# Kernel tuning notes

Measured on AMD Instinct MI355X. Metric: run time of the kernel, lower is better.

Reference implementation:

```python
import jax, jax.numpy as jnp
import numpy as np

WP = 1.0     # warp_penalty
TEMP = 0.01  # soft-min temperature
BIG = 1e7    # finite stand-in for +inf (exp(-BIG/TEMP) == 0 exactly in fp32)


def setup_inputs() -> dict:
    key = jax.random.key(0)
    k1, k2, k3, k4 = jax.random.split(key, 4)
    B, T1, T2, C = 8, 256, 1024, 128
    fea_a = jax.random.normal(k1, (B, T1, C), jnp.float32)
    fea_b = jax.random.normal(k2, (B, T2, C), jnp.float32)
    len_a = jax.random.randint(k3, (B,), T1 // 2, T1 + 1)
    len_b = jax.random.randint(k4, (B,), T2 // 2, T2 + 1)
    return {"fea_a": fea_a, "len_a": len_a, "fea_b": fea_b, "len_b": len_b}


def _softmin(v, temp):
    # v: [3, B, T1]; stable -temp*log(sum(exp(-v/temp)))
    m = jnp.min(v, axis=0)
    return m - temp * jnp.log(jnp.sum(jnp.exp(-(v - m) / temp), axis=0))


def _soft_dtw(fea_a, fea_b, len_a, len_b, wp=WP, temp=TEMP):
    B, T1, C = fea_a.shape
    T2 = fea_b.shape[1]
    # L1 cost: [B, T2, T1]  (rows index fea_b, cols index fea_a, as in torch code)
    cost = jnp.mean(jnp.abs(fea_a[:, None, :, :] - fea_b[:, :, None, :]), axis=-1)
    # skewed cost: skew[b, d, j] = cost[b, clip(d-j, 0, T2-1), j]
    D = T1 + T2 - 1
    d = jnp.arange(D)[:, None]
    j = jnp.arange(T1)[None, :]
    idx = jnp.clip(d - j, 0, T2 - 1)           # [D, T1]
    skew = cost[:, idx, j]                      # [B, D, T1]
    skew = jnp.swapaxes(skew, 0, 1)             # [D, B, T1] for scan

    pc0 = jnp.full((B, T1 + 1), BIG, jnp.float32)       # path_cost (diag d-1)
    pcp0 = pc0.at[:, 0].set(0.0)                         # path_cost_prev (diag d-2)

    def step(carry, crow):
        pc, pcp = carry
        dirs = jnp.stack([pcp[:, :-1], pc[:, 1:] + wp, pc[:, :-1] + wp], axis=0)
        new = crow + _softmin(dirs, temp)                # [B, T1]
        new = jnp.concatenate([jnp.full((B, 1), BIG, new.dtype), new], axis=1)
        return (new, pc), new

    _, ys = jax.lax.scan(step, (pc0, pcp0), skew)        # ys: [D, B, T1+1]
    # per-sample answer: diagonal len_a+len_b-2, entry len_a
    di = len_a + len_b - 2
    loss_i = ys[di, jnp.arange(B), len_a]
    return jnp.sum(loss_i)  # reduction='mean' over a length-1 accumulator == sum


def reference(fea_a, len_a, fea_b, len_b):
    return _soft_dtw(fea_a, fea_b, len_a, len_b)
```

## Files before the change

kernel.cpp:

```cpp
#include <hip/hip_runtime.h>
#include <hip/hip_bf16.h>
#include <hip/hip_fp16.h>
#include <cstddef>
#include <cstdint>

#define BIGV 10000000.0f
#define WPV  1.0f

#define BATCH 8
#define T1N 256
#define T2N 1024
#define CN 128
#define DN 1279

#define RPB 16
#define NSLOT 3
#define SLOT_BYTES (RPB * 1024)
#define FLAG_MAGIC 0x600D0000

typedef __attribute__((ext_vector_type(2))) _Float16 half2v;

__global__ __launch_bounds__(256) void cost_kernel(const float* __restrict__ A,
                                                   const float* __restrict__ Bf,
                                                   const int* __restrict__ lenA,
                                                   const int* __restrict__ lenB,
                                                   float* __restrict__ sk) {
    __shared__ char As[64 * 256];
    __shared__ char Bs[127 * 256];

    const int b  = blockIdx.z;
    const int d0 = blockIdx.y * 64;
    const int j0 = blockIdx.x * 64;
    const int tid = threadIdx.x;

    const int dEnd = lenA[b] + lenB[b] - 2;
    if (d0 > dEnd) return;

    const float* Ab = A  + (size_t)b * T1N * CN;
    const float* Bb = Bf + (size_t)b * T2N * CN;

    const int tj = tid & 15;
    const int td = tid >> 4;
    const int brow0 = td - tj + 63;
    const int rbase = d0 - j0 - 63;

#define SWB(row, g) (((row) << 8) + ((((g) + (row)) & 15) << 4))

    #pragma unroll
    for (int i = 0; i < 8; ++i) {
        int idx = tid + i * 256;
        int row = idx >> 5;
        int q   = idx & 31;
        float4 f = *(const float4*)(Ab + (size_t)(j0 + row) * CN + (q << 2));
        half2v h0 = { (_Float16)f.x, (_Float16)f.y };
        half2v h1 = { (_Float16)f.z, (_Float16)f.w };
        char* dst = As + SWB(row, q >> 1) + ((q & 1) << 3);
        ((uint32_t*)dst)[0] = __builtin_bit_cast(uint32_t, h0);
        ((uint32_t*)dst)[1] = __builtin_bit_cast(uint32_t, h1);
    }
    #pragma unroll
    for (int i = 0; i < 16; ++i) {
        int idx = tid + i * 256;
        if (idx < 4064) {
            int row = idx >> 5;
            int q   = idx & 31;
            int gr = rbase + row;
            gr = gr < 0 ? 0 : (gr > T2N - 1 ? T2N - 1 : gr);
            float4 f = *(const float4*)(Bb + (size_t)gr * CN + (q << 2));
            half2v h0 = { (_Float16)f.x, (_Float16)f.y };
            half2v h1 = { (_Float16)f.z, (_Float16)f.w };
            char* dst = Bs + SWB(row, q >> 1) + ((q & 1) << 3);
            ((uint32_t*)dst)[0] = __builtin_bit_cast(uint32_t, h0);
            ((uint32_t*)dst)[1] = __builtin_bit_cast(uint32_t, h1);
        }
    }
    __syncthreads();

    float acc[4][4];
    #pragma unroll
    for (int i = 0; i < 4; ++i)
        #pragma unroll
        for (int j = 0; j < 4; ++j) acc[i][j] = 0.0f;

    const half2v one2 = { (_Float16)1.0f, (_Float16)1.0f };

    for (int g = 0; g < 16; ++g) {
        uint4 a4[4], bv[7];
        #pragma unroll
        for (int ji = 0; ji < 4; ++ji) {
            int row = tj + 16 * ji;
            a4[ji] = *(const uint4*)(As + SWB(row, g));
        }
        #pragma unroll
        for (int m = 0; m < 7; ++m) {
            int row = brow0 + 16 * (m - 3);
            bv[m] = *(const uint4*)(Bs + SWB(row, g));
        }
        #pragma unroll
        for (int dk = 0; dk < 4; ++dk) {
            #pragma unroll
            for (int ji = 0; ji < 4; ++ji) {
                uint4 au = a4[ji];
                uint4 bu = bv[dk - ji + 3];
                float a = acc[dk][ji];
                #pragma unroll
                for (int w = 0; w < 4; ++w) {
                    uint32_t ua = (&au.x)[w];
                    uint32_t ub = (&bu.x)[w];
                    half2v d2 = __builtin_bit_cast(half2v, ua)
                              - __builtin_bit_cast(half2v, ub);
                    uint32_t du = __builtin_bit_cast(uint32_t, d2) & 0x7FFF7FFFu;
#if __has_builtin(__builtin_amdgcn_fdot2)
                    a = __builtin_amdgcn_fdot2(__builtin_bit_cast(half2v, du),
                                               one2, a, false);
#else
                    half2v ad = __builtin_bit_cast(half2v, du);
                    a += (float)ad.x + (float)ad.y;
#endif
                }
                acc[dk][ji] = a;
            }
        }
    }
#undef SWB

    #pragma unroll
    for (int dk = 0; dk < 4; ++dk) {
        int d = d0 + td + 16 * dk;
        if (d < DN) {
            size_t rowoff = ((size_t)b * DN + d) * T1N;
            #pragma unroll
            for (int ji = 0; ji < 4; ++ji) {
                int j = j0 + tj + 16 * ji;
                sk[rowoff + j] = acc[dk][ji] * (1.0f / 128.0f);
            }
        }
    }
}

__global__ __launch_bounds__(128, 1) void dp_wave_kernel(const float* __restrict__ sk,
                                                         const int* __restrict__ lenA,
                                                         const int* __restrict__ lenB,
                                                         float* __restrict__ partials,
                                                         int* __restrict__ flags,
                                                         float* __restrict__ out) {
    __shared__ char ring[NSLOT * SLOT_BYTES];
    __shared__ int prod_cnt;
    __shared__ int cons_cnt;

    const int b = blockIdx.x;
    if (threadIdx.x == 0) { prod_cnt = 0; cons_cnt = 0; }
    __syncthreads();

    const int wave = threadIdx.x >> 6;
    const int L = threadIdx.x & 63;

    const int la = __builtin_amdgcn_readfirstlane(lenA[b]);
    const int lb = __builtin_amdgcn_readfirstlane(lenB[b]);
    const int dEnd = la + lb - 2;
    const int kLast = dEnd >> 4;
    const int nblk = kLast + 1;

    if (wave == 1) {
        const float* skbp = sk + (size_t)b * DN * T1N + (L << 2);
        for (int k = 0; k < nblk; ++k) {
            if (k >= NSLOT) {
                while (__hip_atomic_load(&cons_cnt, __ATOMIC_ACQUIRE,
                                         __HIP_MEMORY_SCOPE_WORKGROUP) < k - (NSLOT - 1))
                    __builtin_amdgcn_s_sleep(1);
            }
            char* slot = ring + (k % NSLOT) * SLOT_BYTES;
            const int r0 = k * RPB;
            #pragma unroll
            for (int r = 0; r < RPB; ++r) {
                int row = r0 + r; row = row > DN - 1 ? DN - 1 : row;
                __builtin_amdgcn_global_load_lds(
                    (const __attribute__((address_space(1))) void*)(skbp + (size_t)row * T1N),
                    (__attribute__((address_space(3))) void*)(slot + (r << 10)),
                    16, 0, 0);
            }
            asm volatile("s_waitcnt vmcnt(16)" ::: "memory");
            if (L == 0)
                __hip_atomic_store(&prod_cnt, k, __ATOMIC_RELEASE,
                                   __HIP_MEMORY_SCOPE_WORKGROUP);
        }
        asm volatile("s_waitcnt vmcnt(0)" ::: "memory");
        if (L == 0)
            __hip_atomic_store(&prod_cnt, nblk, __ATOMIC_RELEASE,
                               __HIP_MEMORY_SCOPE_WORKGROUP);
        return;
    }

    float v1_0 = BIGV, v1_1 = BIGV, v1_2 = BIGV, v1_3 = BIGV;
    float v2_0 = BIGV, v2_1 = BIGV, v2_2 = BIGV, v2_3 = BIGV;
    float p1_prev = (L == 0) ? 0.0f : BIGV;

#define SHFL_UP1(SRC)                                                       \
    __int_as_float(__builtin_amdgcn_update_dpp(                             \
        __float_as_int(BIGV), __float_as_int(SRC),                          \
        0x138 , 0xF, 0xF, false))

#define DP_STEP(C4) do {                                                    \
        float4 c = (C4);                                                    \
        float p1 = SHFL_UP1(v1_3);                                          \
        float p2 = p1_prev;                                                 \
        float n0 = c.x + fminf(p2,   fminf(v1_0, p1)   + WPV);              \
        float n1 = c.y + fminf(v2_0, fminf(v1_1, v1_0) + WPV);              \
        float n2 = c.z + fminf(v2_1, fminf(v1_2, v1_1) + WPV);              \
        float n3 = c.w + fminf(v2_2, fminf(v1_3, v1_2) + WPV);              \
        p1_prev = p1;                                                       \
        v2_0 = v1_0; v2_1 = v1_1; v2_2 = v1_2; v2_3 = v1_3;                 \
        v1_0 = n0;   v1_1 = n1;   v1_2 = n2;   v1_3 = n3;                   \
    } while (0)

#define DP_STEP_G(C4, R) do {                                               \
        float4 c = (C4);                                                    \
        float p1 = SHFL_UP1(v1_3);                                          \
        float p2 = p1_prev;                                                 \
        float n0 = c.x + fminf(p2,   fminf(v1_0, p1)   + WPV);              \
        float n1 = c.y + fminf(v2_0, fminf(v1_1, v1_0) + WPV);              \
        float n2 = c.z + fminf(v2_1, fminf(v1_2, v1_1) + WPV);              \
        float n3 = c.w + fminf(v2_2, fminf(v1_3, v1_2) + WPV);              \
        if ((R) <= rem) {                                                   \
            p1_prev = p1;                                                   \
            v2_0 = v1_0; v2_1 = v1_1; v2_2 = v1_2; v2_3 = v1_3;             \
            v1_0 = n0;   v1_1 = n1;   v1_2 = n2;   v1_3 = n3;               \
        }                                                                   \
    } while (0)

#define WAIT_BLK(K) do {                                                    \
        while (__hip_atomic_load(&prod_cnt, __ATOMIC_ACQUIRE,               \
                                 __HIP_MEMORY_SCOPE_WORKGROUP) < (K) + 1)   \
            __builtin_amdgcn_s_sleep(1);                                    \
    } while (0)

#define READ_BLK(K)                                                         \
        const char* slot = ring + ((K) % NSLOT) * SLOT_BYTES;               \
        const float4* rp = (const float4*)(slot + (L << 4));                \
        float4 c0  = rp[0 * 64],  c1  = rp[1 * 64],  c2  = rp[2 * 64],  c3  = rp[3 * 64];  \
        float4 c4_ = rp[4 * 64],  c5  = rp[5 * 64],  c6  = rp[6 * 64],  c7  = rp[7 * 64];  \
        float4 c8  = rp[8 * 64],  c9  = rp[9 * 64],  c10 = rp[10 * 64], c11 = rp[11 * 64]; \
        float4 c12 = rp[12 * 64], c13 = rp[13 * 64], c14 = rp[14 * 64], c15 = rp[15 * 64]; \
        __builtin_amdgcn_sched_barrier(0);

    for (int k = 0; k < kLast; ++k) {
        WAIT_BLK(k);
        READ_BLK(k);
        DP_STEP(c0);  DP_STEP(c1);  DP_STEP(c2);  DP_STEP(c3);
        DP_STEP(c4_); DP_STEP(c5);  DP_STEP(c6);  DP_STEP(c7);
        DP_STEP(c8);  DP_STEP(c9);  DP_STEP(c10); DP_STEP(c11);
        DP_STEP(c12); DP_STEP(c13); DP_STEP(c14); DP_STEP(c15);
        if (L == 0)
            __hip_atomic_store(&cons_cnt, k + 1, __ATOMIC_RELEASE,
                               __HIP_MEMORY_SCOPE_WORKGROUP);
    }

    {
        const int rem = dEnd & 15;
        WAIT_BLK(kLast);
        READ_BLK(kLast);
        DP_STEP_G(c0, 0);   DP_STEP_G(c1, 1);   DP_STEP_G(c2, 2);   DP_STEP_G(c3, 3);
        DP_STEP_G(c4_, 4);  DP_STEP_G(c5, 5);   DP_STEP_G(c6, 6);   DP_STEP_G(c7, 7);
        DP_STEP_G(c8, 8);   DP_STEP_G(c9, 9);   DP_STEP_G(c10, 10); DP_STEP_G(c11, 11);
        DP_STEP_G(c12, 12); DP_STEP_G(c13, 13); DP_STEP_G(c14, 14); DP_STEP_G(c15, 15);
    }

    const int tcap = la - 1;
    if (L == (tcap >> 2)) {
        const int k = tcap & 3;
        float r = v1_0;
        if (k == 1) r = v1_1;
        else if (k == 2) r = v1_2;
        else if (k == 3) r = v1_3;
        partials[b] = r;
        __threadfence();
        __hip_atomic_store(&flags[b], FLAG_MAGIC + b,
                           __ATOMIC_RELEASE, __HIP_MEMORY_SCOPE_AGENT);
    }

    if (b == 0 && L == 0) {
        float s = 0.0f;
        for (int i = 0; i < BATCH; ++i) {
            while (__hip_atomic_load(&flags[i], __ATOMIC_ACQUIRE,
                                     __HIP_MEMORY_SCOPE_AGENT) != FLAG_MAGIC + i)
                __builtin_amdgcn_s_sleep(2);
            s += __hip_atomic_load(&partials[i], __ATOMIC_RELAXED,
                                   __HIP_MEMORY_SCOPE_AGENT);
        }
        out[0] = s;
    }
#undef READ_BLK
#undef WAIT_BLK
#undef DP_STEP_G
#undef DP_STEP
#undef SHFL_UP1
}

extern "C" void kernel_launch(void* const* d_in, const int* in_sizes, int n_in,
                              void* d_out, int out_size, void* d_ws, size_t ws_size,
                              hipStream_t stream) {
    const float* feaA = (const float*)d_in[0];
    const int*   lenA = (const int*)d_in[1];
    const float* feaB = (const float*)d_in[2];
    const int*   lenB = (const int*)d_in[3];

    float* sk = (float*)d_ws;
    float* partials = (float*)((char*)d_ws + (size_t)BATCH * DN * T1N * sizeof(float));
    int*   flags    = (int*)(partials + BATCH);

    cost_kernel<<<dim3(T1N / 64, (DN + 63) / 64, BATCH), 256, 0, stream>>>(feaA, feaB, lenA, lenB, sk);
    dp_wave_kernel<<<BATCH, 128, 0, stream>>>(sk, lenA, lenB, partials, flags, (float*)d_out);
}
```

Before: 144.7 us.

## Fuse cost and DP kernels into one persistent kernel with per-tile readiness counters

Merges the cost-matrix kernel and the wavefront DP kernel into a single launch. Eight blocks run the DP while 248 worker blocks compute 64x64 cost tiles in diagonal-major order and bump per-(batch, diagonal-block) atomic counters. The DP producer wave spins on those counters before streaming rows, so the DP can start while later cost tiles are still being computed. In exchange it adds a memset, global atomics, threadfences and spin-waiting. It also depends on the DP blocks and the workers being co-resident, since the DP blocks wait on tiles the workers produce.

```diff
diff --git a/kernel.cpp b/kernel.cpp
--- a/kernel.cpp
+++ b/kernel.cpp
@@ -12,148 +12,166 @@
 #define T2N 1024
 #define CN 128
 #define DN 1279
+#define NDT 20
+#define NTILE 640
+#define NWORK 248
 
 #define RPB 16
 #define NSLOT 3
 #define SLOT_BYTES (RPB * 1024)
 #define FLAG_MAGIC 0x600D0000
+#define LDS_BYTES 86016
 
 typedef __attribute__((ext_vector_type(2))) _Float16 half2v;
 
-__global__ __launch_bounds__(256) void cost_kernel(const float* __restrict__ A,
-                                                   const float* __restrict__ Bf,
-                                                   const int* __restrict__ lenA,
-                                                   const int* __restrict__ lenB,
-                                                   float* __restrict__ sk) {
-    __shared__ char As[64 * 256];
-    __shared__ char Bs[127 * 256];
-
-    const int b  = blockIdx.z;
-    const int d0 = blockIdx.y * 64;
-    const int j0 = blockIdx.x * 64;
-    const int tid = threadIdx.x;
-
-    const int dEnd = lenA[b] + lenB[b] - 2;
-    if (d0 > dEnd) return;
-
-    const float* Ab = A  + (size_t)b * T1N * CN;
-    const float* Bb = Bf + (size_t)b * T2N * CN;
-
-    const int tj = tid & 15;
-    const int td = tid >> 4;
-    const int brow0 = td - tj + 63;
-    const int rbase = d0 - j0 - 63;
+__global__ __launch_bounds__(256, 1) void fused_kernel(const float* __restrict__ A,
+                                                       const float* __restrict__ Bf,
+                                                       const int* __restrict__ lenA,
+                                                       const int* __restrict__ lenB,
+                                                       float* __restrict__ sk,
+                                                       int* __restrict__ cnt,
+                                                       float* __restrict__ partials,
+                                                       int* __restrict__ flags,
+                                                       float* __restrict__ out) {
+    __shared__ __align__(16) char lds[LDS_BYTES];
+
+    const int bid = blockIdx.x;
+
+    if (bid >= BATCH) {
+        char* As = lds;
+        char* Bs = lds + 16384;
+        const int tid = threadIdx.x;
+        const int tj = tid & 15;
+        const int td = tid >> 4;
 
 #define SWB(row, g) (((row) << 8) + ((((g) + (row)) & 15) << 4))
 
-    #pragma unroll
-    for (int i = 0; i < 8; ++i) {
-        int idx = tid + i * 256;
-        int row = idx >> 5;
-        int q   = idx & 31;
-        float4 f = *(const float4*)(Ab + (size_t)(j0 + row) * CN + (q << 2));
-        half2v h0 = { (_Float16)f.x, (_Float16)f.y };
-        half2v h1 = { (_Float16)f.z, (_Float16)f.w };
-        char* dst = As + SWB(row, q >> 1) + ((q & 1) << 3);
-        ((uint32_t*)dst)[0] = __builtin_bit_cast(uint32_t, h0);
-        ((uint32_t*)dst)[1] = __builtin_bit_cast(uint32_t, h1);
-    }
-    #pragma unroll
-    for (int i = 0; i < 16; ++i) {
-        int idx = tid + i * 256;
-        if (idx < 4064) {
-            int row = idx >> 5;
-            int q   = idx & 31;
-            int gr = rbase + row;
-            gr = gr < 0 ? 0 : (gr > T2N - 1 ? T2N - 1 : gr);
-            float4 f = *(const float4*)(Bb + (size_t)gr * CN + (q << 2));
-            half2v h0 = { (_Float16)f.x, (_Float16)f.y };
-            half2v h1 = { (_Float16)f.z, (_Float16)f.w };
-            char* dst = Bs + SWB(row, q >> 1) + ((q & 1) << 3);
-            ((uint32_t*)dst)[0] = __builtin_bit_cast(uint32_t, h0);
-            ((uint32_t*)dst)[1] = __builtin_bit_cast(uint32_t, h1);
+        for (int t = bid - BATCH; t < NTILE; t += NWORK) {
+            const int y  = t >> 5;
+            const int b  = (t >> 2) & 7;
+            const int jb = t & 3;
+            const int d0 = y * 64;
+            const int j0 = jb * 64;
+
+            const int dEnd = lenA[b] + lenB[b] - 2;
+            if (d0 > dEnd) {
+                if (tid == 0)
+                    __hip_atomic_fetch_add(&cnt[b * NDT + y], 1,
+                                           __ATOMIC_RELEASE, __HIP_MEMORY_SCOPE_AGENT);
+                continue;
+            }
+
+            const float* Ab = A  + (size_t)b * T1N * CN;
+            const float* Bb = Bf + (size_t)b * T2N * CN;
+            const int brow0 = td - tj + 63;
+            const int rbase = d0 - j0 - 63;
+
+            #pragma unroll
+            for (int i = 0; i < 8; ++i) {
+                int idx = tid + i * 256;
+                int row = idx >> 5;
+                int q   = idx & 31;
+                float4 f = *(const float4*)(Ab + (size_t)(j0 + row) * CN + (q << 2));
+                half2v h0 = { (_Float16)f.x, (_Float16)f.y };
+                half2v h1 = { (_Float16)f.z, (_Float16)f.w };
+                char* dst = As + SWB(row, q >> 1) + ((q & 1) << 3);
+                ((uint32_t*)dst)[0] = __builtin_bit_cast(uint32_t, h0);
+                ((uint32_t*)dst)[1] = __builtin_bit_cast(uint32_t, h1);
+            }
+            #pragma unroll
+            for (int i = 0; i < 16; ++i) {
+                int idx = tid + i * 256;
+                if (idx < 4064) {
+                    int row = idx >> 5;
+                    int q   = idx & 31;
+                    int gr = rbase + row;
+                    gr = gr < 0 ? 0 : (gr > T2N - 1 ? T2N - 1 : gr);
+                    float4 f = *(const float4*)(Bb + (size_t)gr * CN + (q << 2));
+                    half2v h0 = { (_Float16)f.x, (_Float16)f.y };
+                    half2v h1 = { (_Float16)f.z, (_Float16)f.w };
+                    char* dst = Bs + SWB(row, q >> 1) + ((q & 1) << 3);
+                    ((uint32_t*)dst)[0] = __builtin_bit_cast(uint32_t, h0);
+                    ((uint32_t*)dst)[1] = __builtin_bit_cast(uint32_t, h1);
+                }
+            }
+            __syncthreads();
+
+            float acc[4][4];
+            #pragma unroll
+            for (int i = 0; i < 4; ++i)
+                #pragma unroll
+                for (int j = 0; j < 4; ++j) acc[i][j] = 0.0f;
+
+            const half2v one2 = { (_Float16)1.0f, (_Float16)1.0f };
+
+            for (int g = 0; g < 16; ++g) {
+                uint4 a4[4], bv[7];
+                #pragma unroll
+                for (int ji = 0; ji < 4; ++ji)
+                    a4[ji] = *(const uint4*)(As + SWB(tj + 16 * ji, g));
+                #pragma unroll
+                for (int m = 0; m < 7; ++m)
+                    bv[m] = *(const uint4*)(Bs + SWB(brow0 + 16 * (m - 3), g));
+                #pragma unroll
+                for (int dk = 0; dk < 4; ++dk) {
+                    #pragma unroll
+                    for (int ji = 0; ji < 4; ++ji) {
+                        uint4 au = a4[ji];
+                        uint4 bu = bv[dk - ji + 3];
+                        float a = acc[dk][ji];
+                        #pragma unroll
+                        for (int w = 0; w < 4; ++w) {
+                            half2v d2 = __builtin_bit_cast(half2v, (&au.x)[w])
+                                      - __builtin_bit_cast(half2v, (&bu.x)[w]);
+                            uint32_t du = __builtin_bit_cast(uint32_t, d2) & 0x7FFF7FFFu;
+#if __has_builtin(__builtin_amdgcn_fdot2)
+                            a = __builtin_amdgcn_fdot2(__builtin_bit_cast(half2v, du),
+                                                       one2, a, false);
+#else
+                            half2v ad = __builtin_bit_cast(half2v, du);
+                            a += (float)ad.x + (float)ad.y;
+#endif
+                        }
+                        acc[dk][ji] = a;
+                    }
+                }
+            }
+
+            #pragma unroll
+            for (int dk = 0; dk < 4; ++dk) {
+                int d = d0 + td + 16 * dk;
+                if (d < DN) {
+                    size_t rowoff = ((size_t)b * DN + d) * T1N;
+                    #pragma unroll
+                    for (int ji = 0; ji < 4; ++ji) {
+                        int j = j0 + tj + 16 * ji;
+                        sk[rowoff + j] = acc[dk][ji] * (1.0f / 128.0f);
+                    }
+                }
+            }
+
+            __threadfence();
+            __syncthreads();
+            if (tid == 0)
+                __hip_atomic_fetch_add(&cnt[b * NDT + y], 1,
+                                       __ATOMIC_RELEASE, __HIP_MEMORY_SCOPE_AGENT);
+            __syncthreads();
         }
-    }
-    __syncthreads();
-
-    float acc[4][4];
-    #pragma unroll
-    for (int i = 0; i < 4; ++i)
-        #pragma unroll
-        for (int j = 0; j < 4; ++j) acc[i][j] = 0.0f;
-
-    const half2v one2 = { (_Float16)1.0f, (_Float16)1.0f };
-
-    for (int g = 0; g < 16; ++g) {
-        uint4 a4[4], bv[7];
-        #pragma unroll
-        for (int ji = 0; ji < 4; ++ji) {
-            int row = tj + 16 * ji;
-            a4[ji] = *(const uint4*)(As + SWB(row, g));
-        }
-        #pragma unroll
-        for (int m = 0; m < 7; ++m) {
-            int row = brow0 + 16 * (m - 3);
-            bv[m] = *(const uint4*)(Bs + SWB(row, g));
-        }
-        #pragma unroll
-        for (int dk = 0; dk < 4; ++dk) {
-            #pragma unroll
-            for (int ji = 0; ji < 4; ++ji) {
-                uint4 au = a4[ji];
-                uint4 bu = bv[dk - ji + 3];
-                float a = acc[dk][ji];
-                #pragma unroll
-                for (int w = 0; w < 4; ++w) {
-                    uint32_t ua = (&au.x)[w];
-                    uint32_t ub = (&bu.x)[w];
-                    half2v d2 = __builtin_bit_cast(half2v, ua)
-                              - __builtin_bit_cast(half2v, ub);
-                    uint32_t du = __builtin_bit_cast(uint32_t, d2) & 0x7FFF7FFFu;
-#if __has_builtin(__builtin_amdgcn_fdot2)
-                    a = __builtin_amdgcn_fdot2(__builtin_bit_cast(half2v, du),
-                                               one2, a, false);
-#else
-                    half2v ad = __builtin_bit_cast(half2v, du);
-                    a += (float)ad.x + (float)ad.y;
-#endif
-                }
-                acc[dk][ji] = a;
-            }
-        }
-    }
 #undef SWB
-
-    #pragma unroll
-    for (int dk = 0; dk < 4; ++dk) {
-        int d = d0 + td + 16 * dk;
-        if (d < DN) {
-            size_t rowoff = ((size_t)b * DN + d) * T1N;
-            #pragma unroll
-            for (int ji = 0; ji < 4; ++ji) {
-                int j = j0 + tj + 16 * ji;
-                sk[rowoff + j] = acc[dk][ji] * (1.0f / 128.0f);
-            }
-        }
-    }
-}
-
-__global__ __launch_bounds__(128, 1) void dp_wave_kernel(const float* __restrict__ sk,
-                                                         const int* __restrict__ lenA,
-                                                         const int* __restrict__ lenB,
-                                                         float* __restrict__ partials,
-                                                         int* __restrict__ flags,
-                                                         float* __restrict__ out) {
-    __shared__ char ring[NSLOT * SLOT_BYTES];
-    __shared__ int prod_cnt;
-    __shared__ int cons_cnt;
-
-    const int b = blockIdx.x;
-    if (threadIdx.x == 0) { prod_cnt = 0; cons_cnt = 0; }
+        return;
+    }
+
+    char* ring = lds;
+    int* prod_cnt = (int*)(lds + NSLOT * SLOT_BYTES);
+    int* cons_cnt = prod_cnt + 1;
+
+    const int b = bid;
+    if (threadIdx.x == 0) { *prod_cnt = 0; *cons_cnt = 0; }
     __syncthreads();
 
     const int wave = threadIdx.x >> 6;
     const int L = threadIdx.x & 63;
+    if (wave >= 2) return;
 
     const int la = __builtin_amdgcn_readfirstlane(lenA[b]);
     const int lb = __builtin_amdgcn_readfirstlane(lenB[b]);
@@ -162,10 +180,19 @@
     const int nblk = kLast + 1;
 
     if (wave == 1) {
+        const int* cntb = cnt + b * NDT;
         const float* skbp = sk + (size_t)b * DN * T1N + (L << 2);
+        int y_ck = 0;
         for (int k = 0; k < nblk; ++k) {
+            int ygate = k * 16 + 15; if (ygate > dEnd) ygate = dEnd;
+            ygate >>= 6;
+            while (y_ck <= ygate) {
+                if (__hip_atomic_load(&cntb[y_ck], __ATOMIC_ACQUIRE,
+                                      __HIP_MEMORY_SCOPE_AGENT) == 4) ++y_ck;
+                else __builtin_amdgcn_s_sleep(2);
+            }
             if (k >= NSLOT) {
-                while (__hip_atomic_load(&cons_cnt, __ATOMIC_ACQUIRE,
+                while (__hip_atomic_load(cons_cnt, __ATOMIC_ACQUIRE,
                                          __HIP_MEMORY_SCOPE_WORKGROUP) < k - (NSLOT - 1))
                     __builtin_amdgcn_s_sleep(1);
             }
@@ -181,12 +208,12 @@
             }
             asm volatile("s_waitcnt vmcnt(16)" ::: "memory");
             if (L == 0)
-                __hip_atomic_store(&prod_cnt, k, __ATOMIC_RELEASE,
+                __hip_atomic_store(prod_cnt, k, __ATOMIC_RELEASE,
                                    __HIP_MEMORY_SCOPE_WORKGROUP);
         }
         asm volatile("s_waitcnt vmcnt(0)" ::: "memory");
         if (L == 0)
-            __hip_atomic_store(&prod_cnt, nblk, __ATOMIC_RELEASE,
+            __hip_atomic_store(prod_cnt, nblk, __ATOMIC_RELEASE,
                                __HIP_MEMORY_SCOPE_WORKGROUP);
         return;
     }
@@ -229,7 +256,7 @@
     } while (0)
 
 #define WAIT_BLK(K) do {                                                    \
-        while (__hip_atomic_load(&prod_cnt, __ATOMIC_ACQUIRE,               \
+        while (__hip_atomic_load(prod_cnt, __ATOMIC_ACQUIRE,                \
                                  __HIP_MEMORY_SCOPE_WORKGROUP) < (K) + 1)   \
             __builtin_amdgcn_s_sleep(1);                                    \
     } while (0)
@@ -251,7 +278,7 @@
         DP_STEP(c8);  DP_STEP(c9);  DP_STEP(c10); DP_STEP(c11);
         DP_STEP(c12); DP_STEP(c13); DP_STEP(c14); DP_STEP(c15);
         if (L == 0)
-            __hip_atomic_store(&cons_cnt, k + 1, __ATOMIC_RELEASE,
+            __hip_atomic_store(cons_cnt, k + 1, __ATOMIC_RELEASE,
                                __HIP_MEMORY_SCOPE_WORKGROUP);
     }
 
@@ -307,7 +334,10 @@
     float* sk = (float*)d_ws;
     float* partials = (float*)((char*)d_ws + (size_t)BATCH * DN * T1N * sizeof(float));
     int*   flags    = (int*)(partials + BATCH);
-
-    cost_kernel<<<dim3(T1N / 64, (DN + 63) / 64, BATCH), 256, 0, stream>>>(feaA, feaB, lenA, lenB, sk);
-    dp_wave_kernel<<<BATCH, 128, 0, stream>>>(sk, lenA, lenB, partials, flags, (float*)d_out);
+    int*   cnt      = flags + BATCH;
+
+    hipMemsetAsync(cnt, 0, BATCH * NDT * sizeof(int), stream);
+    fused_kernel<<<BATCH + NWORK, 256, 0, stream>>>(feaA, feaB, lenA, lenB,
+                                                    sk, cnt, partials, flags,
+                                                    (float*)d_out);
 }
```

New measurement: 191.5 us. +32.3%, slower.
